# Optimization experiments

Measured on AMD Instinct MI355X. Metric: run time of the kernel, lower is better.

## Reference

```python
import jax, jax.numpy as jnp
import numpy as np

THETA = 1.0
DILATIONS = (1, 2, 3, 4)
EPS = 1e-6


def _scale_features(x, d):
    # x: [B, C, H, W]; one pyramid scale (dilation d)
    B, C, H, W = x.shape
    k = 3 + 2 * (d - 1)          # kernel size per original formula
    pad = d * d                   # pad so effective span d*(k-1)+1 = 2d^2+1 preserves HxW
    K = k * k
    patches = jax.lax.conv_general_dilated_patches(
        x, (k, k), (1, 1), [(pad, pad), (pad, pad)], rhs_dilation=(d, d)
    )  # [B, C*K, H, W], channel-major per input channel
    p = patches.reshape(B, C, K, H, W)

    mu = p.mean(axis=2, keepdims=True)
    diff = p - mu
    var_biased = (diff * diff).mean(axis=2)                 # E[(p-mu)^2]
    std = jnp.sqrt(var_biased * (K / (K - 1))) + EPS        # torch .std is unbiased (ddof=1)

    contrast = var_biased / (std * std)                     # mean(normed^2)
    energy = (p * p).mean(axis=2)
    entropy = -(p * jnp.log(p + EPS)).mean(axis=2)
    # NB: original precedence -> 1.0 / mean(1 + |p - mu|)
    homogeneity = 1.0 / ((1.0 + jnp.abs(diff)).mean(axis=2))

    feats = jnp.stack([contrast, energy, entropy, homogeneity], axis=2)  # [B, C, 4, H, W]
    # martingale transform: exp(theta*log(f+eps) - 0.5*theta^2)
    M = jnp.exp(THETA * jnp.log(feats + EPS) - 0.5 * THETA ** 2)
    return M.reshape(B, C * 4, H, W)  # cat over channels of per-channel feature stacks


def setup_inputs() -> dict:
    key = jax.random.key(0)
    x = jax.random.uniform(key, (2, 4, 256, 256), dtype=jnp.float32)
    return {"x": x}


def reference(x):
    return tuple(_scale_features(x, d) for d in DILATIONS)
```

## Files before the change

### kernel.cpp

```cpp
#include <hip/hip_runtime.h>
#include <cstddef>

#define EPS 1e-6f
constexpr float INV_SQRT_E = 0.6065306597126334f;

template <int D>
__device__ __forceinline__ void body(const float* __restrict__ x,
                                     float* __restrict__ out,
                                     char* smem, int bc, int H, int W)
{
    constexpr int PAD = D * D;
    constexpr int KS  = 2 * D + 1;
    constexpr int K   = KS * KS;
    constexpr int TW  = 64, TH = 8;
    constexpr int LW  = TW + 2 * PAD;
    constexpr int LH  = TH + 2 * PAD;
    constexpr int NE  = LH * LW;
    constexpr int NI2 = (NE + 1023) / 1024;
    constexpr float INVK = 1.0f / (float)K;
    constexpr float UNB  = (float)K / (float)(K - 1);

    float*  sx  = (float*)smem;
    float*  slg = sx + NE;
    float2* cs2 = (float2*)(slg + NE);
    float*  cs1 = (float*)(cs2 + TH * LW);
    float*  muP  = (float*)cs2;
    float*  sadP = muP + TH * 64;

    const int w0 = blockIdx.x * TW;
    const int h0 = blockIdx.y * TH;
    const float* xp = x + (size_t)bc * H * W;
    const int tid = threadIdx.y * 64 + threadIdx.x;

    float v0b[NI2], v1b[NI2];
    #pragma unroll
    for (int i = 0; i < NI2; ++i) {
        const int e0 = 2 * (tid + i * 512);
        float v0 = 0.0f, v1 = 0.0f;
        if (e0 < NE) {
            const int r  = e0 / LW;
            const int cc = e0 - r * LW;
            const int gh = h0 - PAD + r;
            const int gw = w0 - PAD + cc;
            if (gh >= 0 && gh < H) {
                if constexpr ((PAD & 1) == 0) {
                    if (gw >= 0 && gw + 1 < W) {
                        const float2 v = *(const float2*)&xp[gh * W + gw];
                        v0 = v.x; v1 = v.y;
                    } else {
                        if (gw >= 0 && gw < W)         v0 = xp[gh * W + gw];
                        if (gw + 1 >= 0 && gw + 1 < W) v1 = xp[gh * W + gw + 1];
                    }
                } else {
                    if (gw >= 0 && gw < W)         v0 = xp[gh * W + gw];
                    if (gw + 1 >= 0 && gw + 1 < W) v1 = xp[gh * W + gw + 1];
                }
            }
        }
        v0b[i] = v0; v1b[i] = v1;
    }
    #pragma unroll
    for (int i = 0; i < NI2; ++i) {
        const int e0 = 2 * (tid + i * 512);
        if (e0 < NE) {
            *(float2*)&sx[e0]  = make_float2(v0b[i], v1b[i]);
            *(float2*)&slg[e0] = make_float2(v0b[i] * __logf(v0b[i] + EPS),
                                             v1b[i] * __logf(v1b[i] + EPS));
        }
    }
    __syncthreads();

    const int tx = threadIdx.x;
    const int ty = threadIdx.y;

    if constexpr (K <= 9) {
        const float* bx = sx  + ty * LW + tx;
        const float* bl = slg + ty * LW + tx;
        float s = 0.f, s2 = 0.f, sl = 0.f, ta[K];
        #pragma unroll
        for (int mi = 0; mi < KS; ++mi)
            #pragma unroll
            for (int mj = 0; mj < KS; ++mj) {
                const float v = bx[mi * LW + mj];
                ta[mi * KS + mj] = v;
                s  += v;
                s2  = fmaf(v, v, s2);
                sl += bl[mi * LW + mj];
            }
        const float mu = s * INVK;
        float sad = 0.f;
        #pragma unroll
        for (int i = 0; i < K; ++i) sad += fabsf(ta[i] - mu);

        const float energy   = s2 * INVK;
        const float var      = fmaxf(energy - mu * mu, 0.f);
        const float sd       = sqrtf(var * UNB) + EPS;
        const float contrast = var / (sd * sd);
        const float entropy  = -sl * INVK;
        const float homog    = 1.f / (1.f + sad * INVK);
        const size_t fs = (size_t)H * W;
        const size_t ro = (size_t)(h0 + ty) * W;
        float* op = out + (size_t)bc * 4 * fs + w0 + tx;
        __builtin_nontemporal_store((contrast + EPS) * INV_SQRT_E, &op[0 * fs + ro]);
        __builtin_nontemporal_store((energy   + EPS) * INV_SQRT_E, &op[1 * fs + ro]);
        __builtin_nontemporal_store((entropy  + EPS) * INV_SQRT_E, &op[2 * fs + ro]);
        __builtin_nontemporal_store((homog    + EPS) * INV_SQRT_E, &op[3 * fs + ro]);
        return;
    } else {
        constexpr int HW2 = LW / 2;
        if (tid < 4 * HW2) {
            const int p  = tid / HW2;
            const int c2 = (tid - p * HW2) * 2;
            if (!(D == 3 && p == 3)) {
                const int vA = (D == 2) ? ((p < 2) ? p : p + 2) : p;
                const int vB = vA + D;
                const float2* cx = (const float2*)(sx + vA * LW + c2);
                float sA0=0,sA1=0,qA0=0,qA1=0,sB0=0,sB1=0,qB0=0,qB1=0;
                #pragma unroll
                for (int t = 0; t <= KS; ++t) {
                    const float2 v = cx[t * D * HW2];
                    if (t < KS) { sA0 += v.x; sA1 += v.y;
                                  qA0 = fmaf(v.x,v.x,qA0); qA1 = fmaf(v.y,v.y,qA1); }
                    if (t >= 1) { sB0 += v.x; sB1 += v.y;
                                  qB0 = fmaf(v.x,v.x,qB0); qB1 = fmaf(v.y,v.y,qB1); }
                }
                const float2* cl = (const float2*)(slg + vA * LW + c2);
                float lA0=0,lA1=0,lB0=0,lB1=0;
                #pragma unroll
                for (int t = 0; t <= KS; ++t) {
                    const float2 g = cl[t * D * HW2];
                    if (t < KS) { lA0 += g.x; lA1 += g.y; }
                    if (t >= 1) { lB0 += g.x; lB1 += g.y; }
                }
                *(float4*)&cs2[vA * LW + c2] = make_float4(sA0, qA0, sA1, qA1);
                *(float4*)&cs2[vB * LW + c2] = make_float4(sB0, qB0, sB1, qB1);
                *(float2*)&cs1[vA * LW + c2] = make_float2(lA0, lA1);
                *(float2*)&cs1[vB * LW + c2] = make_float2(lB0, lB1);
            } else {
                #pragma unroll
                for (int rr = 6; rr <= 7; ++rr) {
                    const float2* cx = (const float2*)(sx  + rr * LW + c2);
                    const float2* cl = (const float2*)(slg + rr * LW + c2);
                    float s0=0,s1=0,q0=0,q1=0,l0=0,l1=0;
                    #pragma unroll
                    for (int mi = 0; mi < KS; ++mi) {
                        const float2 v = cx[mi * D * HW2];
                        const float2 g = cl[mi * D * HW2];
                        s0 += v.x; s1 += v.y;
                        q0 = fmaf(v.x,v.x,q0); q1 = fmaf(v.y,v.y,q1);
                        l0 += g.x; l1 += g.y;
                    }
                    *(float4*)&cs2[rr * LW + c2] = make_float4(s0, q0, s1, q1);
                    *(float2*)&cs1[rr * LW + c2] = make_float2(l0, l1);
                }
            }
        }
        __syncthreads();

        float s = 0.f, s2 = 0.f, sl = 0.f;
        const float2* q2 = cs2 + ty * LW + tx;
        const float*  q1 = cs1 + ty * LW + tx;
        #pragma unroll
        for (int mj = 0; mj < KS; ++mj) {
            const float2 q = q2[mj * D];
            s += q.x; s2 += q.y; sl += q1[mj * D];
        }
        const float mu = s * INVK;
        __syncthreads();

        muP[ty * 64 + tx] = mu;
        __syncthreads();

        if (ty < 4) {
            const int o = ty;
            if (!(D == 3 && o == 3)) {
                const int rA = (D == 2) ? ((o < 2) ? o : o + 2) : o;
                const int rB = rA + D;
                const float muA = muP[rA * 64 + tx];
                const float muB = muP[rB * 64 + tx];
                float sadA = 0.f, sadB = 0.f;
                const float* bp = sx + rA * LW + tx;
                #pragma unroll
                for (int mj = 0; mj < KS; ++mj) {
                    const float* cp = bp + mj * D;
                    #pragma unroll
                    for (int t = 0; t <= KS; ++t) {
                        const float v = cp[t * D * LW];
                        if (t < KS) sadA += fabsf(v - muA);
                        if (t >= 1) sadB += fabsf(v - muB);
                    }
                }
                sadP[rA * 64 + tx] = sadA;
                sadP[rB * 64 + tx] = sadB;
            } else {
                #pragma unroll
                for (int rr = 6; rr <= 7; ++rr) {
                    const float mur = muP[rr * 64 + tx];
                    const float* bp = sx + rr * LW + tx;
                    float sd = 0.f;
                    #pragma unroll
                    for (int mi = 0; mi < KS; ++mi)
                        #pragma unroll
                        for (int mj = 0; mj < KS; ++mj)
                            sd += fabsf(bp[mi * D * LW + mj * D] - mur);
                    sadP[rr * 64 + tx] = sd;
                }
            }
        }
        __syncthreads();
        const float sad = sadP[ty * 64 + tx];

        const float energy   = s2 * INVK;
        const float var      = fmaxf(energy - mu * mu, 0.f);
        const float sd       = sqrtf(var * UNB) + EPS;
        const float contrast = var / (sd * sd);
        const float entropy  = -sl * INVK;
        const float homog    = 1.f / (1.f + sad * INVK);
        const size_t fs = (size_t)H * W;
        const size_t ro = (size_t)(h0 + ty) * W;
        float* op = out + (size_t)bc * 4 * fs + w0 + tx;
        __builtin_nontemporal_store((contrast + EPS) * INV_SQRT_E, &op[0 * fs + ro]);
        __builtin_nontemporal_store((energy   + EPS) * INV_SQRT_E, &op[1 * fs + ro]);
        __builtin_nontemporal_store((entropy  + EPS) * INV_SQRT_E, &op[2 * fs + ro]);
        __builtin_nontemporal_store((homog    + EPS) * INV_SQRT_E, &op[3 * fs + ro]);
    }
}

__global__ __launch_bounds__(512, 8) void tex_fused(
    const float* __restrict__ x, float* __restrict__ out, int H, int W)
{
    extern __shared__ __align__(16) char smem[];
    const int dz = blockIdx.z & 3;
    const int bc = blockIdx.z >> 2;
    const size_t per = (size_t)8 * 4 * H * W;
    switch (dz) {
        case 0: body<4>(x, out + 3 * per, smem, bc, H, W); break;
        case 1: body<3>(x, out + 2 * per, smem, bc, H, W); break;
        case 2: body<2>(x, out + 1 * per, smem, bc, H, W); break;
        default: body<1>(x, out + 0 * per, smem, bc, H, W); break;
    }
}

extern "C" void kernel_launch(void* const* d_in, const int* in_sizes, int n_in,
                              void* d_out, int out_size, void* d_ws, size_t ws_size,
                              hipStream_t stream) {
    const float* x = (const float*)d_in[0];
    float* out = (float*)d_out;

    const int H = 256, W = 256;
    const size_t smem_bytes = 39936;

    dim3 blk(64, 8, 1);
    dim3 grd(W / 64, H / 8, 8 * 4);
    tex_fused<<<grd, blk, smem_bytes, stream>>>(x, out, H, W);
}
```

Before: 77.32 us.

## Drop staged log tile, pad LDS rows, share SAD loads across column pairs

Stops staging x*log(x+eps) in shared memory. The entropy term is now recomputed from the x tile wherever it is consumed, which shrinks LDS use and should allow more blocks per CU. LDS rows are padded for D=2 and D=4 to avoid bank conflicts. For even dilations the SAD pass is regrouped so each thread handles a 2x2 group of outputs and reuses the loaded values across two columns. In exchange, the log is evaluated redundantly in several threads, and the SAD work for even D is concentrated in fewer warps.

```diff
diff --git a/kernel.cpp b/kernel.cpp
--- a/kernel.cpp
+++ b/kernel.cpp
@@ -13,16 +13,17 @@
     constexpr int KS  = 2 * D + 1;
     constexpr int K   = KS * KS;
     constexpr int TW  = 64, TH = 8;
-    constexpr int LW  = TW + 2 * PAD;
+    constexpr int LWD = TW + 2 * PAD;
+    constexpr int BPAD = (D == 4) ? 4 : ((D == 2) ? 2 : 0);
+    constexpr int LW  = LWD + BPAD;
     constexpr int LH  = TH + 2 * PAD;
-    constexpr int NE  = LH * LW;
-    constexpr int NI2 = (NE + 1023) / 1024;
+    constexpr int NED = LH * LWD;
+    constexpr int NI2 = (NED + 1023) / 1024;
     constexpr float INVK = 1.0f / (float)K;
     constexpr float UNB  = (float)K / (float)(K - 1);
 
     float*  sx  = (float*)smem;
-    float*  slg = sx + NE;
-    float2* cs2 = (float2*)(slg + NE);
+    float2* cs2 = (float2*)(sx + LH * LW);
     float*  cs1 = (float*)(cs2 + TH * LW);
     float*  muP  = (float*)cs2;
     float*  sadP = muP + TH * 64;
@@ -37,9 +38,9 @@
     for (int i = 0; i < NI2; ++i) {
         const int e0 = 2 * (tid + i * 512);
         float v0 = 0.0f, v1 = 0.0f;
-        if (e0 < NE) {
-            const int r  = e0 / LW;
-            const int cc = e0 - r * LW;
+        if (e0 < NED) {
+            const int r  = e0 / LWD;
+            const int cc = e0 - r * LWD;
             const int gh = h0 - PAD + r;
             const int gw = w0 - PAD + cc;
             if (gh >= 0 && gh < H) {
@@ -62,10 +63,10 @@
     #pragma unroll
     for (int i = 0; i < NI2; ++i) {
         const int e0 = 2 * (tid + i * 512);
-        if (e0 < NE) {
-            *(float2*)&sx[e0]  = make_float2(v0b[i], v1b[i]);
-            *(float2*)&slg[e0] = make_float2(v0b[i] * __logf(v0b[i] + EPS),
-                                             v1b[i] * __logf(v1b[i] + EPS));
+        if (e0 < NED) {
+            const int r  = e0 / LWD;
+            const int cc = e0 - r * LWD;
+            *(float2*)&sx[r * LW + cc] = make_float2(v0b[i], v1b[i]);
         }
     }
     __syncthreads();
@@ -74,9 +75,8 @@
     const int ty = threadIdx.y;
 
     if constexpr (K <= 9) {
-        const float* bx = sx  + ty * LW + tx;
-        const float* bl = slg + ty * LW + tx;
-        float s = 0.f, s2 = 0.f, sl = 0.f, ta[K];
+        const float* bx = sx + ty * LW + tx;
+        float s = 0.f, s2 = 0.f, ta[K];
         #pragma unroll
         for (int mi = 0; mi < KS; ++mi)
             #pragma unroll
@@ -85,13 +85,14 @@
                 ta[mi * KS + mj] = v;
                 s  += v;
                 s2  = fmaf(v, v, s2);
-                sl += bl[mi * LW + mj];
             }
         const float mu = s * INVK;
-        float sad = 0.f;
+        float sad = 0.f, sl = 0.f;
         #pragma unroll
-        for (int i = 0; i < K; ++i) sad += fabsf(ta[i] - mu);
-
+        for (int i = 0; i < K; ++i) {
+            sad += fabsf(ta[i] - mu);
+            sl  += ta[i] * __logf(ta[i] + EPS);
+        }
         const float energy   = s2 * INVK;
         const float var      = fmaxf(energy - mu * mu, 0.f);
         const float sd       = sqrtf(var * UNB) + EPS;
@@ -107,30 +108,27 @@
         __builtin_nontemporal_store((homog    + EPS) * INV_SQRT_E, &op[3 * fs + ro]);
         return;
     } else {
-        constexpr int HW2 = LW / 2;
-        if (tid < 4 * HW2) {
-            const int p  = tid / HW2;
-            const int c2 = (tid - p * HW2) * 2;
+        constexpr int HPAIRS = LWD / 2;
+        if (tid < 4 * HPAIRS) {
+            const int p  = tid / HPAIRS;
+            const int c2 = (tid - p * HPAIRS) * 2;
             if (!(D == 3 && p == 3)) {
                 const int vA = (D == 2) ? ((p < 2) ? p : p + 2) : p;
                 const int vB = vA + D;
                 const float2* cx = (const float2*)(sx + vA * LW + c2);
-                float sA0=0,sA1=0,qA0=0,qA1=0,sB0=0,sB1=0,qB0=0,qB1=0;
+                float sA0=0,sA1=0,qA0=0,qA1=0,lA0=0,lA1=0;
+                float sB0=0,sB1=0,qB0=0,qB1=0,lB0=0,lB1=0;
                 #pragma unroll
                 for (int t = 0; t <= KS; ++t) {
-                    const float2 v = cx[t * D * HW2];
+                    const float2 v = cx[t * D * (LW / 2)];
+                    const float g0 = v.x * __logf(v.x + EPS);
+                    const float g1 = v.y * __logf(v.y + EPS);
                     if (t < KS) { sA0 += v.x; sA1 += v.y;
-                                  qA0 = fmaf(v.x,v.x,qA0); qA1 = fmaf(v.y,v.y,qA1); }
+                                  qA0 = fmaf(v.x,v.x,qA0); qA1 = fmaf(v.y,v.y,qA1);
+                                  lA0 += g0; lA1 += g1; }
                     if (t >= 1) { sB0 += v.x; sB1 += v.y;
-                                  qB0 = fmaf(v.x,v.x,qB0); qB1 = fmaf(v.y,v.y,qB1); }
-                }
-                const float2* cl = (const float2*)(slg + vA * LW + c2);
-                float lA0=0,lA1=0,lB0=0,lB1=0;
-                #pragma unroll
-                for (int t = 0; t <= KS; ++t) {
-                    const float2 g = cl[t * D * HW2];
-                    if (t < KS) { lA0 += g.x; lA1 += g.y; }
-                    if (t >= 1) { lB0 += g.x; lB1 += g.y; }
+                                  qB0 = fmaf(v.x,v.x,qB0); qB1 = fmaf(v.y,v.y,qB1);
+                                  lB0 += g0; lB1 += g1; }
                 }
                 *(float4*)&cs2[vA * LW + c2] = make_float4(sA0, qA0, sA1, qA1);
                 *(float4*)&cs2[vB * LW + c2] = make_float4(sB0, qB0, sB1, qB1);
@@ -139,16 +137,15 @@
             } else {
                 #pragma unroll
                 for (int rr = 6; rr <= 7; ++rr) {
-                    const float2* cx = (const float2*)(sx  + rr * LW + c2);
-                    const float2* cl = (const float2*)(slg + rr * LW + c2);
+                    const float2* cx = (const float2*)(sx + rr * LW + c2);
                     float s0=0,s1=0,q0=0,q1=0,l0=0,l1=0;
                     #pragma unroll
                     for (int mi = 0; mi < KS; ++mi) {
-                        const float2 v = cx[mi * D * HW2];
-                        const float2 g = cl[mi * D * HW2];
+                        const float2 v = cx[mi * D * (LW / 2)];
                         s0 += v.x; s1 += v.y;
                         q0 = fmaf(v.x,v.x,q0); q1 = fmaf(v.y,v.y,q1);
-                        l0 += g.x; l1 += g.y;
+                        l0 += v.x * __logf(v.x + EPS);
+                        l1 += v.y * __logf(v.y + EPS);
                     }
                     *(float4*)&cs2[rr * LW + c2] = make_float4(s0, q0, s1, q1);
                     *(float2*)&cs1[rr * LW + c2] = make_float2(l0, l1);
@@ -171,39 +168,82 @@
         muP[ty * 64 + tx] = mu;
         __syncthreads();
 
-        if (ty < 4) {
-            const int o = ty;
-            if (!(D == 3 && o == 3)) {
-                const int rA = (D == 2) ? ((o < 2) ? o : o + 2) : o;
+        if constexpr ((D & 1) == 0) {
+            if (ty < 2) {
+                const int p = ty * 2 + (tx >> 5);
+                const int g = tx & 31;
+                const int rA = (D == 2) ? ((p < 2) ? p : p + 2) : p;
                 const int rB = rA + D;
-                const float muA = muP[rA * 64 + tx];
-                const float muB = muP[rB * 64 + tx];
-                float sadA = 0.f, sadB = 0.f;
-                const float* bp = sx + rA * LW + tx;
+                const int cA = (D == 2) ? (4 * (g >> 1) + (g & 1))
+                                        : (8 * (g >> 2) + (g & 3));
+                const int cB = cA + D;
+                const float m00 = muP[rA * 64 + cA], m01 = muP[rA * 64 + cB];
+                const float m10 = muP[rB * 64 + cA], m11 = muP[rB * 64 + cB];
+                float a00 = 0.f, a01 = 0.f, a10 = 0.f, a11 = 0.f;
+                const float* bp = sx + rA * LW + cA;
                 #pragma unroll
-                for (int mj = 0; mj < KS; ++mj) {
-                    const float* cp = bp + mj * D;
+                for (int t = 0; t <= KS; ++t) {
+                    const float v = bp[t * D * LW];
+                    if (t < KS) a00 += fabsf(v - m00);
+                    if (t >= 1) a10 += fabsf(v - m10);
+                }
+                #pragma unroll 1
+                for (int m = 1; m < KS; ++m) {
+                    const float* cp = bp + m * D;
                     #pragma unroll
                     for (int t = 0; t <= KS; ++t) {
                         const float v = cp[t * D * LW];
-                        if (t < KS) sadA += fabsf(v - muA);
-                        if (t >= 1) sadB += fabsf(v - muB);
-                    }
-                }
-                sadP[rA * 64 + tx] = sadA;
-                sadP[rB * 64 + tx] = sadB;
-            } else {
-                #pragma unroll
-                for (int rr = 6; rr <= 7; ++rr) {
-                    const float mur = muP[rr * 64 + tx];
-                    const float* bp = sx + rr * LW + tx;
-                    float sd = 0.f;
-                    #pragma unroll
-                    for (int mi = 0; mi < KS; ++mi)
+                        if (t < KS) { a00 += fabsf(v - m00); a01 += fabsf(v - m01); }
+                        if (t >= 1) { a10 += fabsf(v - m10); a11 += fabsf(v - m11); }
+                    }
+                }
+                {
+                    const float* cp = bp + KS * D;
+                    #pragma unroll
+                    for (int t = 0; t <= KS; ++t) {
+                        const float v = cp[t * D * LW];
+                        if (t < KS) a01 += fabsf(v - m01);
+                        if (t >= 1) a11 += fabsf(v - m11);
+                    }
+                }
+                sadP[rA * 64 + cA] = a00; sadP[rA * 64 + cB] = a01;
+                sadP[rB * 64 + cA] = a10; sadP[rB * 64 + cB] = a11;
+            }
+        } else {
+            if (ty < 4) {
+                const int o = ty;
+                if (o != 3) {
+                    const int rA = o;
+                    const int rB = rA + D;
+                    const float muA = muP[rA * 64 + tx];
+                    const float muB = muP[rB * 64 + tx];
+                    float sadA = 0.f, sadB = 0.f;
+                    const float* bp = sx + rA * LW + tx;
+                    #pragma unroll
+                    for (int mj = 0; mj < KS; ++mj) {
+                        const float* cp = bp + mj * D;
                         #pragma unroll
-                        for (int mj = 0; mj < KS; ++mj)
-                            sd += fabsf(bp[mi * D * LW + mj * D] - mur);
-                    sadP[rr * 64 + tx] = sd;
+                        for (int t = 0; t <= KS; ++t) {
+                            const float v = cp[t * D * LW];
+                            if (t < KS) sadA += fabsf(v - muA);
+                            if (t >= 1) sadB += fabsf(v - muB);
+                        }
+                    }
+                    sadP[rA * 64 + tx] = sadA;
+                    sadP[rB * 64 + tx] = sadB;
+                } else {
+                    #pragma unroll
+                    for (int rr = 6; rr <= 7; ++rr) {
+                        const float mur = muP[rr * 64 + tx];
+                        const float* bp = sx + rr * LW + tx;
+                        float sd = 0.f;
+                        #pragma unroll
+                        for (int mi = 0; mi < KS; ++mi)
+                            #pragma unroll
+                            for (int mj = 0; mj < KS; ++mj)
+                                sd += fabsf(bp[mi * D * LW + mj * D] - mur);
+                        sadP[rr * 64 + tx] = sd;
+                    }
                 }
             }
         }
@@ -248,7 +288,7 @@
     float* out = (float*)d_out;
 
     const int H = 256, W = 256;
-    const size_t smem_bytes = 39936;
+    const size_t smem_bytes = 25600;
 
     dim3 blk(64, 8, 1);
     dim3 grd(W / 64, H / 8, 8 * 4);
```

After: 85.51 us. 1.11x slower.
